# Kernel optimization log

Measured on AMD Instinct MI355X. Metric: run time of the kernel, lower is better.

Reference implementation:

```python
import jax, jax.numpy as jnp
import numpy as np

D_MODEL = 768
N_HEADS = 12
HEAD_DIM = D_MODEL // N_HEADS


def setup_inputs() -> dict:
    key = jax.random.key(0)
    ks = jax.random.split(key, 9)
    s = 1.0 / np.sqrt(D_MODEL)
    inp = {
        "inputs": jax.random.normal(ks[0], (1, 4096, D_MODEL), dtype=jnp.float32),
        "Wq": jax.random.uniform(ks[1], (D_MODEL, D_MODEL), jnp.float32, -s, s),
        "bq": jax.random.uniform(ks[2], (D_MODEL,), jnp.float32, -s, s),
        "Wk": jax.random.uniform(ks[3], (D_MODEL, D_MODEL), jnp.float32, -s, s),
        "bk": jax.random.uniform(ks[4], (D_MODEL,), jnp.float32, -s, s),
        "Wv": jax.random.uniform(ks[5], (D_MODEL, D_MODEL), jnp.float32, -s, s),
        "bv": jax.random.uniform(ks[6], (D_MODEL,), jnp.float32, -s, s),
        "Wo": jax.random.uniform(ks[7], (D_MODEL, D_MODEL), jnp.float32, -s, s),
        "bo": jax.random.uniform(ks[8], (D_MODEL,), jnp.float32, -s, s),
    }
    return inp


def reference(inputs, Wq, bq, Wk, bk, Wv, bv, Wo, bo):
    B, S, D = inputs.shape
    H, Hd = N_HEADS, HEAD_DIM

    def split_heads(x):  # [B,S,D] -> [B,H,S,Hd]
        return x.reshape(B, S, H, Hd).transpose(0, 2, 1, 3)

    # nn.Linear computes x @ W.T + b
    Q = split_heads(inputs @ Wq.T + bq)
    K = split_heads(inputs @ Wk.T + bk)
    V = split_heads(inputs @ Wv.T + bv)

    scores = jnp.einsum("bhsd,bhtd->bhst", Q, K) / jnp.sqrt(jnp.float32(Hd))
    causal = jnp.tril(jnp.ones((S, S), dtype=bool))  # True = keep
    scores = jnp.where(causal, scores, -jnp.inf)
    attn = jax.nn.softmax(scores, axis=-1)  # dropout is identity in eval

    out = jnp.einsum("bhst,bhtd->bhsd", attn, V)
    out = out.transpose(0, 2, 1, 3).reshape(B, S, D)
    return out @ Wo.T + bo
```

## Files before the change

kernel.cpp:

```cpp
#include <hip/hip_runtime.h>
#include <stdint.h>

#define SEQ 4096
#define DM 768
#define NH 12
#define HD 64

typedef unsigned short u16;
typedef short short8 __attribute__((ext_vector_type(8)));
typedef float floatx4 __attribute__((ext_vector_type(4)));
typedef u16 u16x4 __attribute__((ext_vector_type(4)));

__device__ inline u16 f2b(float f) {
  union { float f; uint32_t u; } v; v.f = f;
  uint32_t u = v.u;
  return (u16)((u + 0x7fffu + ((u >> 16) & 1u)) >> 16);
}

__device__ inline float b2f(u16 x) {
  union { uint32_t u; float f; } v; v.u = ((uint32_t)x) << 16;
  return v.f;
}

#if defined(__has_builtin)
#if __has_builtin(__builtin_amdgcn_cvt_pk_bf16_f32)
#define HAVE_PK_BF16 1
#endif
#endif

__device__ inline uint32_t pk_bf16(float a, float b) {
#ifdef HAVE_PK_BF16
  typedef __bf16 bf16x2_t __attribute__((ext_vector_type(2)));
  union { bf16x2_t v; uint32_t u; } c;
  c.v = __builtin_amdgcn_cvt_pk_bf16_f32(a, b);
  return c.u;
#else
  return (uint32_t)f2b(a) | ((uint32_t)f2b(b) << 16);
#endif
}

__device__ inline void load_lds16(const void* g, void* l) {
  __builtin_amdgcn_global_load_lds(
      (const __attribute__((address_space(1))) uint32_t*)g,
      (__attribute__((address_space(3))) uint32_t*)l, 16, 0, 0);
}

__global__ __launch_bounds__(256) void convert_all(
    const float* __restrict__ X, const float* __restrict__ Wq,
    const float* __restrict__ Wk, const float* __restrict__ Wv,
    const float* __restrict__ Wo,
    u16* __restrict__ Xb, u16* __restrict__ Wqb, u16* __restrict__ Wkb,
    u16* __restrict__ Wvb, u16* __restrict__ Wob) {
  int t = blockIdx.x * 256 + threadIdx.x;
  const int NX = SEQ * DM / 4;
  const int NW = DM * DM / 4;
  const float* src; u16* dst; int off;
  if (t < NX)               { src = X;  dst = Xb;  off = t; }
  else if (t < NX + NW)     { src = Wq; dst = Wqb; off = t - NX; }
  else if (t < NX + 2 * NW) { src = Wk; dst = Wkb; off = t - NX - NW; }
  else if (t < NX + 3 * NW) { src = Wv; dst = Wvb; off = t - NX - 2 * NW; }
  else if (t < NX + 4 * NW) { src = Wo; dst = Wob; off = t - NX - 3 * NW; }
  else return;
  float4 v = *(const float4*)(src + (size_t)off * 4);
  uint2 o;
  o.x = pk_bf16(v.x, v.y);
  o.y = pk_bf16(v.z, v.w);
  *(uint2*)(dst + (size_t)off * 4) = o;
}

__global__ __launch_bounds__(256) void gemm_qkv(
    const u16* __restrict__ Xb,
    const u16* __restrict__ Wqb, const u16* __restrict__ Wkb,
    const u16* __restrict__ Wvb,
    const float* __restrict__ bq, const float* __restrict__ bk,
    const float* __restrict__ bv,
    u16* __restrict__ Qh, u16* __restrict__ Kh, u16* __restrict__ VtG) {
  const u16* W; const float* bias;
  const int z = blockIdx.z;
  if (z == 0)      { W = Wqb; bias = bq; }
  else if (z == 1) { W = Wkb; bias = bk; }
  else             { W = Wvb; bias = bv; }

  __shared__ u16 smem[32768];

  const int tid = threadIdx.x;
  const int wave = tid >> 6, lane = tid & 63;
  const int g = lane >> 4, ln = lane & 15;
  const int m0 = blockIdx.y * 128, n0 = blockIdx.x * 128;
  const int wm = (wave & 1) * 64, wn = (wave >> 1) * 64;
  const int srow = lane >> 3;
  const int schunk = (lane & 7) ^ srow;
  const int swz = ln & 7;

  floatx4 acc[4][4] = {};

#pragma unroll
  for (int i = 0; i < 4; ++i) {
    int u = wave * 4 + i;
    load_lds16(Xb + (size_t)(m0 + u * 8 + srow) * DM + schunk * 8, smem + u * 512);
    load_lds16(W + (size_t)(n0 + u * 8 + srow) * DM + schunk * 8,
               smem + 16384 + u * 512);
  }

  for (int kt = 0; kt < 12; ++kt) {
    const int cur = kt & 1;
    __syncthreads();
    if (kt < 11) {
      const int k0 = (kt + 1) * 64, nb = cur ^ 1;
#pragma unroll
      for (int i = 0; i < 4; ++i) {
        int u = wave * 4 + i;
        load_lds16(Xb + (size_t)(m0 + u * 8 + srow) * DM + k0 + schunk * 8,
                   smem + nb * 8192 + u * 512);
        load_lds16(W + (size_t)(n0 + u * 8 + srow) * DM + k0 + schunk * 8,
                   smem + 16384 + nb * 8192 + u * 512);
      }
    }
    const u16* Ac = smem + cur * 8192;
    const u16* Bc = smem + 16384 + cur * 8192;
    short8 af[4][2], bf[4][2];
#pragma unroll
    for (int mi = 0; mi < 4; ++mi)
#pragma unroll
      for (int kh = 0; kh < 2; ++kh)
        af[mi][kh] = *(const short8*)(Ac + (wm + mi * 16 + ln) * 64 +
                                      ((kh * 4 + g) ^ swz) * 8);
#pragma unroll
    for (int ni = 0; ni < 4; ++ni)
#pragma unroll
      for (int kh = 0; kh < 2; ++kh)
        bf[ni][kh] = *(const short8*)(Bc + (wn + ni * 16 + ln) * 64 +
                                      ((kh * 4 + g) ^ swz) * 8);
#pragma unroll
    for (int kh = 0; kh < 2; ++kh)
#pragma unroll
      for (int mi = 0; mi < 4; ++mi)
#pragma unroll
        for (int ni = 0; ni < 4; ++ni)
          acc[mi][ni] = __builtin_amdgcn_mfma_f32_16x16x32_bf16(
              af[mi][kh], bf[ni][kh], acc[mi][ni], 0, 0, 0);
  }

  const float qscale = 0.125f * 1.44269504089f;
  __syncthreads();

  if (z == 2) {
#pragma unroll
    for (int mi = 0; mi < 4; ++mi) {
      int row0 = wm + mi * 16 + g * 4;
#pragma unroll
      for (int ni = 0; ni < 4; ++ni) {
        int col = wn + ni * 16 + ln;
        float b = bias[n0 + col];
        uint2 o;
        o.x = pk_bf16(acc[mi][ni][0] + b, acc[mi][ni][1] + b);
        o.y = pk_bf16(acc[mi][ni][2] + b, acc[mi][ni][3] + b);
        *(uint2*)(smem + col * 136 + row0) = o;
      }
    }
    __syncthreads();
#pragma unroll
    for (int t = 0; t < 8; ++t) {
      int unit = tid + t * 256;
      int dcol = unit >> 4, ch = unit & 15;
      short8 v = *(const short8*)(smem + dcol * 136 + ch * 8);
      int col = n0 + dcol, hh = col >> 6, dd = col & 63;
      *(short8*)(VtG + ((size_t)(hh * 64 + dd)) * SEQ + m0 + ch * 8) = v;
    }
  } else {
    u16* out = (z == 0) ? Qh : Kh;
    float cs = (z == 0) ? qscale : 1.0f;
#pragma unroll
    for (int mi = 0; mi < 4; ++mi) {
      int row0 = wm + mi * 16 + g * 4;
#pragma unroll
      for (int ni = 0; ni < 4; ++ni) {
        int col = wn + ni * 16 + ln;
        float b = bias[n0 + col];
        uint32_t w0 = pk_bf16((acc[mi][ni][0] + b) * cs, (acc[mi][ni][1] + b) * cs);
        uint32_t w1 = pk_bf16((acc[mi][ni][2] + b) * cs, (acc[mi][ni][3] + b) * cs);
        smem[(row0 + 0) * 136 + col] = (u16)w0;
        smem[(row0 + 1) * 136 + col] = (u16)(w0 >> 16);
        smem[(row0 + 2) * 136 + col] = (u16)w1;
        smem[(row0 + 3) * 136 + col] = (u16)(w1 >> 16);
      }
    }
    __syncthreads();
#pragma unroll
    for (int t = 0; t < 8; ++t) {
      int unit = tid + t * 256;
      int row = unit >> 4, ch = unit & 15;
      short8 v = *(const short8*)(smem + row * 136 + ch * 8);
      int col = n0 + ch * 8, hh = col >> 6, dd = col & 63;
      *(short8*)(out + ((size_t)hh * SEQ + m0 + row) * HD + dd) = v;
    }
  }
}

#define CHUNK 16
__global__ __launch_bounds__(256) void attn_chunk(
    const u16* __restrict__ Qh, const u16* __restrict__ Kh,
    const u16* __restrict__ VtG, u16* __restrict__ Opart,
    float2* __restrict__ Mlp) {
  const int h = blockIdx.x;
  const int b = blockIdx.y;
  int qb, ci;
  if (b < 16)      { qb = b;               ci = 0; }
  else if (b < 48) { int r = b - 16; qb = 16 + (r >> 1); ci = r & 1; }
  else if (b < 96) { int r = b - 48; int d = r / 3; qb = 32 + d; ci = r - d * 3; }
  else             { int r = b - 96; qb = 48 + (r >> 2); ci = r & 3; }
  const int kb0 = ci * CHUNK;
  const int kb1 = min(kb0 + CHUNK, qb + 1);

  const int tid = threadIdx.x, wave = tid >> 6, lane = tid & 63;
  const int g = lane >> 4, ln = lane & 15;
  const int q0 = qb * 64;
  const int srow = lane >> 3;
  const int schunk = (lane & 7) ^ srow;
  const int swz = ln & 7;

  __shared__ u16 Ks[4096];
  __shared__ u16 Vt[4096];
  __shared__ u16 Ps[4][16 * 72];

  const u16* Qbase = Qh + ((size_t)h * SEQ + q0 + wave * 16 + ln) * HD;
  short8 aq[2] = { *(const short8*)(Qbase + g * 8),
                   *(const short8*)(Qbase + 32 + g * 8) };

  floatx4 oacc[4] = {};
  float m_i = -1e30f, l_i = 0.f;
  u16* PsW = &Ps[wave][0];

  const size_t kbase = (size_t)h * SEQ * HD;
  const size_t vbase = (size_t)h * 64 * SEQ;

  for (int kb = kb0; kb < kb1; ++kb) {
    __syncthreads();
#pragma unroll
    for (int i = 0; i < 2; ++i) {
      int u = wave * 2 + i;
      load_lds16(Kh + kbase + (size_t)(kb * 64 + u * 8 + srow) * HD + schunk * 8,
                 Ks + u * 512);
      load_lds16(VtG + vbase + (size_t)(u * 8 + srow) * SEQ + kb * 64 + schunk * 8,
                 Vt + u * 512);
    }
    __syncthreads();

    floatx4 st[4] = {};
#pragma unroll
    for (int kh = 0; kh < 2; ++kh)
#pragma unroll
      for (int nt = 0; nt < 4; ++nt) {
        short8 kf = *(const short8*)(Ks + (nt * 16 + ln) * 64 +
                                     ((kh * 4 + g) ^ swz) * 8);
        st[nt] = __builtin_amdgcn_mfma_f32_16x16x32_bf16(kf, aq[kh], st[nt], 0, 0, 0);
      }

    if (kb == qb) {
      int qlocal = wave * 16 + ln;
#pragma unroll
      for (int nt = 0; nt < 4; ++nt)
#pragma unroll
        for (int r = 0; r < 4; ++r)
          if (nt * 16 + g * 4 + r > qlocal) st[nt][r] = -1e30f;
    }

    float mx = -1e30f;
#pragma unroll
    for (int nt = 0; nt < 4; ++nt)
#pragma unroll
      for (int r = 0; r < 4; ++r) mx = fmaxf(mx, st[nt][r]);
    mx = fmaxf(mx, __shfl_xor(mx, 16));
    mx = fmaxf(mx, __shfl_xor(mx, 32));
    float mnew = fmaxf(m_i, mx);
    float alpha = __builtin_amdgcn_exp2f(m_i - mnew);
    m_i = mnew;
    float rs = 0.f;
#pragma unroll
    for (int nt = 0; nt < 4; ++nt)
#pragma unroll
      for (int r = 0; r < 4; ++r) {
        float e = __builtin_amdgcn_exp2f(st[nt][r] - mnew);
        st[nt][r] = e;
        rs += e;
      }
    rs += __shfl_xor(rs, 16);
    rs += __shfl_xor(rs, 32);
    l_i = l_i * alpha + rs;
#pragma unroll
    for (int nt = 0; nt < 4; ++nt) oacc[nt] *= alpha;

#pragma unroll
    for (int nt = 0; nt < 4; ++nt) {
      uint2 pk;
      pk.x = pk_bf16(st[nt][0], st[nt][1]);
      pk.y = pk_bf16(st[nt][2], st[nt][3]);
      *(uint2*)(PsW + ln * 72 + nt * 16 + g * 4) = pk;
    }

#pragma unroll
    for (int ks = 0; ks < 2; ++ks) {
      short8 ap = *(const short8*)(PsW + ln * 72 + ks * 32 + g * 8);
#pragma unroll
      for (int nt = 0; nt < 4; ++nt) {
        short8 vf = *(const short8*)(Vt + (nt * 16 + ln) * 64 +
                                     ((ks * 4 + g) ^ swz) * 8);
        oacc[nt] = __builtin_amdgcn_mfma_f32_16x16x32_bf16(vf, ap, oacc[nt], 0, 0, 0);
      }
    }
  }

  const int slot = (h * 64 + qb) * 4 + ci;
  float inv = 1.f / l_i;
  int qloc = wave * 16 + ln;
  u16* Op = Opart + (size_t)slot * 4096 + qloc * 64;
#pragma unroll
  for (int nt = 0; nt < 4; ++nt) {
    uint2 o;
    o.x = pk_bf16(oacc[nt][0] * inv, oacc[nt][1] * inv);
    o.y = pk_bf16(oacc[nt][2] * inv, oacc[nt][3] * inv);
    *(uint2*)(Op + nt * 16 + g * 4) = o;
  }
  if (g == 0) Mlp[slot * 64 + qloc] = make_float2(m_i, l_i);
}

__global__ __launch_bounds__(256) void attn_merge(
    const u16* __restrict__ Opart, const float2* __restrict__ Mlp,
    u16* __restrict__ Ob) {
  const int h = blockIdx.x, qb = blockIdx.y;
  const int n = (qb >> 4) + 1;
  const int base = (h * 64 + qb) * 4;
  const int tid = threadIdx.x;
  const int q = tid >> 2, d0 = (tid & 3) * 16;

  float m[4], l[4];
  float M = -1e30f;
  for (int i = 0; i < n; ++i) {
    float2 ml = Mlp[(base + i) * 64 + q];
    m[i] = ml.x; l[i] = ml.y;
    M = fmaxf(M, m[i]);
  }
  float w[4], L = 0.f;
  for (int i = 0; i < n; ++i) {
    w[i] = l[i] * __builtin_amdgcn_exp2f(m[i] - M);
    L += w[i];
  }
  float invL = 1.f / L;

  float acc[16];
#pragma unroll
  for (int j = 0; j < 16; ++j) acc[j] = 0.f;
  for (int i = 0; i < n; ++i) {
    float wi = w[i] * invL;
    const u16* src = Opart + (size_t)(base + i) * 4096 + q * 64 + d0;
    short8 a = *(const short8*)(src);
    short8 b = *(const short8*)(src + 8);
#pragma unroll
    for (int j = 0; j < 8; ++j) {
      acc[j]     += wi * b2f((u16)a[j]);
      acc[8 + j] += wi * b2f((u16)b[j]);
    }
  }

  u16* dst = Ob + (size_t)(qb * 64 + q) * DM + h * HD + d0;
#pragma unroll
  for (int j = 0; j < 4; ++j) {
    uint2 o;
    o.x = pk_bf16(acc[j * 4 + 0], acc[j * 4 + 1]);
    o.y = pk_bf16(acc[j * 4 + 2], acc[j * 4 + 3]);
    *(uint2*)(dst + j * 4) = o;
  }
}

__global__ __launch_bounds__(256) void gemm_out(
    const u16* __restrict__ Ab, const u16* __restrict__ Wob,
    const float* __restrict__ bo, float* __restrict__ Cout) {
  __shared__ u16 smem[16384];

  const int tid = threadIdx.x;
  const int wave = tid >> 6, lane = tid & 63;
  const int g = lane >> 4, ln = lane & 15;
  const int m0 = blockIdx.y * 64, n0 = blockIdx.x * 64;
  const int wm = (wave & 1) * 32, wn = (wave >> 1) * 32;
  const int srow = lane >> 3;
  const int schunk = (lane & 7) ^ srow;
  const int swz = ln & 7;

  floatx4 acc[2][2] = {};

#pragma unroll
  for (int i = 0; i < 2; ++i) {
    int u = wave * 2 + i;
    load_lds16(Ab + (size_t)(m0 + u * 8 + srow) * DM + schunk * 8, smem + u * 512);
    load_lds16(Wob + (size_t)(n0 + u * 8 + srow) * DM + schunk * 8,
               smem + 8192 + u * 512);
  }

  for (int kt = 0; kt < 12; ++kt) {
    const int cur = kt & 1;
    __syncthreads();
    if (kt < 11) {
      const int k0 = (kt + 1) * 64, nb = cur ^ 1;
#pragma unroll
      for (int i = 0; i < 2; ++i) {
        int u = wave * 2 + i;
        load_lds16(Ab + (size_t)(m0 + u * 8 + srow) * DM + k0 + schunk * 8,
                   smem + nb * 4096 + u * 512);
        load_lds16(Wob + (size_t)(n0 + u * 8 + srow) * DM + k0 + schunk * 8,
                   smem + 8192 + nb * 4096 + u * 512);
      }
    }
    const u16* Ac = smem + cur * 4096;
    const u16* Bc = smem + 8192 + cur * 4096;
    short8 af[2][2], bf[2][2];
#pragma unroll
    for (int mi = 0; mi < 2; ++mi)
#pragma unroll
      for (int kh = 0; kh < 2; ++kh)
        af[mi][kh] = *(const short8*)(Ac + (wm + mi * 16 + ln) * 64 +
                                      ((kh * 4 + g) ^ swz) * 8);
#pragma unroll
    for (int ni = 0; ni < 2; ++ni)
#pragma unroll
      for (int kh = 0; kh < 2; ++kh)
        bf[ni][kh] = *(const short8*)(Bc + (wn + ni * 16 + ln) * 64 +
                                      ((kh * 4 + g) ^ swz) * 8);
#pragma unroll
    for (int kh = 0; kh < 2; ++kh)
#pragma unroll
      for (int mi = 0; mi < 2; ++mi)
#pragma unroll
        for (int ni = 0; ni < 2; ++ni)
          acc[mi][ni] = __builtin_amdgcn_mfma_f32_16x16x32_bf16(
              af[mi][kh], bf[ni][kh], acc[mi][ni], 0, 0, 0);
  }

#pragma unroll
  for (int mi = 0; mi < 2; ++mi) {
    int row = m0 + wm + mi * 16 + g * 4;
#pragma unroll
    for (int ni = 0; ni < 2; ++ni) {
      int col = n0 + wn + ni * 16 + ln;
      float b = bo[col];
#pragma unroll
      for (int r = 0; r < 4; ++r)
        Cout[(size_t)(row + r) * DM + col] = acc[mi][ni][r] + b;
    }
  }
}

extern "C" void kernel_launch(void* const* d_in, const int* in_sizes, int n_in,
                              void* d_out, int out_size, void* d_ws, size_t ws_size,
                              hipStream_t stream) {
  const float* X  = (const float*)d_in[0];
  const float* Wq = (const float*)d_in[1];
  const float* bq = (const float*)d_in[2];
  const float* Wk = (const float*)d_in[3];
  const float* bk = (const float*)d_in[4];
  const float* Wv = (const float*)d_in[5];
  const float* bv = (const float*)d_in[6];
  const float* Wo = (const float*)d_in[7];
  const float* bo = (const float*)d_in[8];
  float* out = (float*)d_out;

  char* ws = (char*)d_ws;
  u16* Xb  = (u16*)ws; ws += (size_t)SEQ * DM * 2;
  u16* Wqb = (u16*)ws; ws += (size_t)DM * DM * 2;
  u16* Wkb = (u16*)ws; ws += (size_t)DM * DM * 2;
  u16* Wvb = (u16*)ws; ws += (size_t)DM * DM * 2;
  u16* Wob = (u16*)ws; ws += (size_t)DM * DM * 2;
  u16* Qh  = (u16*)ws; ws += (size_t)NH * SEQ * HD * 2;
  u16* Kh  = (u16*)ws; ws += (size_t)NH * SEQ * HD * 2;
  u16* VtG = (u16*)ws; ws += (size_t)NH * SEQ * HD * 2;
  u16* Ob  = (u16*)ws; ws += (size_t)SEQ * DM * 2;
  u16* Opart = (u16*)ws; ws += (size_t)NH * 64 * 4 * 4096 * 2;
  float2* Mlp = (float2*)ws; ws += (size_t)NH * 64 * 4 * 64 * sizeof(float2);

  convert_all<<<5376, 256, 0, stream>>>(X, Wq, Wk, Wv, Wo, Xb, Wqb, Wkb, Wvb, Wob);

  dim3 gq(DM / 128, SEQ / 128, 3);
  gemm_qkv<<<gq, 256, 0, stream>>>(Xb, Wqb, Wkb, Wvb, bq, bk, bv, Qh, Kh, VtG);

  dim3 ga(NH, 160);
  attn_chunk<<<ga, 256, 0, stream>>>(Qh, Kh, VtG, Opart, Mlp);

  dim3 gm(NH, 64);
  attn_merge<<<gm, 256, 0, stream>>>(Opart, Mlp, Ob);

  dim3 go(DM / 64, SEQ / 64);
  gemm_out<<<go, 256, 0, stream>>>(Ob, Wob, bo, out);
}
```

Before: 194.3 us.

## Enlarge attention query tile to 128 rows with 8 waves sharing K/V tiles

The split-K attention kernel now processes 128 query rows per block with 8 waves (512 threads) instead of 64 rows with 4 waves. Each K/V tile loaded into LDS is shared by twice as many queries, so global-to-LDS traffic and block count are halved. Work chunks are now launched in reverse order, heaviest blocks first. Waves whose rows lie entirely before the current key tile skip compute but still join the barriers, so some waves idle on diagonal tiles. The merge kernel is adapted to the 128-row partial layout.

Measured after the change: 200.6 us. 3.3% more time.

```diff
diff --git a/kernel.cpp b/kernel.cpp
--- a/kernel.cpp
+++ b/kernel.cpp
@@ -198,32 +198,34 @@
 }
 
 #define CHUNK 16
-__global__ __launch_bounds__(256) void attn_chunk(
+__global__ __launch_bounds__(512, 8) void attn_chunk(
     const u16* __restrict__ Qh, const u16* __restrict__ Kh,
     const u16* __restrict__ VtG, u16* __restrict__ Opart,
     float2* __restrict__ Mlp) {
   const int h = blockIdx.x;
-  const int b = blockIdx.y;
-  int qb, ci;
-  if (b < 16)      { qb = b;               ci = 0; }
-  else if (b < 48) { int r = b - 16; qb = 16 + (r >> 1); ci = r & 1; }
-  else if (b < 96) { int r = b - 48; int d = r / 3; qb = 32 + d; ci = r - d * 3; }
-  else             { int r = b - 96; qb = 48 + (r >> 2); ci = r & 3; }
+  const int b = 79 - blockIdx.y;
+  int qB, ci;
+  if (b < 8)       { qB = b;               ci = 0; }
+  else if (b < 24) { int r = b - 8;  qB = 8 + (r >> 1); ci = r & 1; }
+  else if (b < 48) { int r = b - 24; int d = r / 3; qB = 16 + d; ci = r - d * 3; }
+  else             { int r = b - 48; qB = 24 + (r >> 2); ci = r & 3; }
   const int kb0 = ci * CHUNK;
-  const int kb1 = min(kb0 + CHUNK, qb + 1);
+  const int kb1 = min(kb0 + CHUNK, 2 * qB + 2);
 
   const int tid = threadIdx.x, wave = tid >> 6, lane = tid & 63;
   const int g = lane >> 4, ln = lane & 15;
-  const int q0 = qb * 64;
+  const int q0 = qB * 128;
+  const int qwave = q0 + wave * 16;
   const int srow = lane >> 3;
   const int schunk = (lane & 7) ^ srow;
   const int swz = ln & 7;
 
   __shared__ u16 Ks[4096];
   __shared__ u16 Vt[4096];
-  __shared__ u16 Ps[4][16 * 72];
-
-  const u16* Qbase = Qh + ((size_t)h * SEQ + q0 + wave * 16 + ln) * HD;
+  __shared__ u16 Ps[8][16 * 72];
+
+  const int qglob = qwave + ln;
+  const u16* Qbase = Qh + ((size_t)h * SEQ + qglob) * HD;
   short8 aq[2] = { *(const short8*)(Qbase + g * 8),
                    *(const short8*)(Qbase + 32 + g * 8) };
 
@@ -236,15 +238,13 @@
 
   for (int kb = kb0; kb < kb1; ++kb) {
     __syncthreads();
-#pragma unroll
-    for (int i = 0; i < 2; ++i) {
-      int u = wave * 2 + i;
-      load_lds16(Kh + kbase + (size_t)(kb * 64 + u * 8 + srow) * HD + schunk * 8,
-                 Ks + u * 512);
-      load_lds16(VtG + vbase + (size_t)(u * 8 + srow) * SEQ + kb * 64 + schunk * 8,
-                 Vt + u * 512);
-    }
-    __syncthreads();
+    load_lds16(Kh + kbase + (size_t)(kb * 64 + wave * 8 + srow) * HD + schunk * 8,
+               Ks + wave * 512);
+    load_lds16(VtG + vbase + (size_t)(wave * 8 + srow) * SEQ + kb * 64 + schunk * 8,
+               Vt + wave * 512);
+    __syncthreads();
+
+    if (kb * 64 > qwave + 15) continue;
 
     floatx4 st[4] = {};
 #pragma unroll
@@ -256,13 +256,12 @@
         st[nt] = __builtin_amdgcn_mfma_f32_16x16x32_bf16(kf, aq[kh], st[nt], 0, 0, 0);
       }
 
-    if (kb == qb) {
-      int qlocal = wave * 16 + ln;
+    if (kb * 64 + 63 > qwave) {
 #pragma unroll
       for (int nt = 0; nt < 4; ++nt)
 #pragma unroll
         for (int r = 0; r < 4; ++r)
-          if (nt * 16 + g * 4 + r > qlocal) st[nt][r] = -1e30f;
+          if (kb * 64 + nt * 16 + g * 4 + r > qglob) st[nt][r] = -1e30f;
     }
 
     float mx = -1e30f;
@@ -310,10 +309,10 @@
     }
   }
 
-  const int slot = (h * 64 + qb) * 4 + ci;
+  const int slot = (h * 32 + qB) * 4 + ci;
   float inv = 1.f / l_i;
   int qloc = wave * 16 + ln;
-  u16* Op = Opart + (size_t)slot * 4096 + qloc * 64;
+  u16* Op = Opart + (size_t)slot * 8192 + qloc * 64;
 #pragma unroll
   for (int nt = 0; nt < 4; ++nt) {
     uint2 o;
@@ -321,22 +320,22 @@
     o.y = pk_bf16(oacc[nt][2] * inv, oacc[nt][3] * inv);
     *(uint2*)(Op + nt * 16 + g * 4) = o;
   }
-  if (g == 0) Mlp[slot * 64 + qloc] = make_float2(m_i, l_i);
+  if (g == 0) Mlp[(size_t)slot * 128 + qloc] = make_float2(m_i, l_i);
 }
 
 __global__ __launch_bounds__(256) void attn_merge(
     const u16* __restrict__ Opart, const float2* __restrict__ Mlp,
     u16* __restrict__ Ob) {
-  const int h = blockIdx.x, qb = blockIdx.y;
-  const int n = (qb >> 4) + 1;
-  const int base = (h * 64 + qb) * 4;
-  const int tid = threadIdx.x;
-  const int q = tid >> 2, d0 = (tid & 3) * 16;
+  const int h = blockIdx.x, qB = blockIdx.y;
+  const int n = (qB >> 3) + 1;
+  const int base = (h * 32 + qB) * 4;
+  const int q = threadIdx.x >> 1;
+  const int d0 = (threadIdx.x & 1) * 32;
 
   float m[4], l[4];
   float M = -1e30f;
   for (int i = 0; i < n; ++i) {
-    float2 ml = Mlp[(base + i) * 64 + q];
+    float2 ml = Mlp[(size_t)(base + i) * 128 + q];
     m[i] = ml.x; l[i] = ml.y;
     M = fmaxf(M, m[i]);
   }
@@ -347,28 +346,29 @@
   }
   float invL = 1.f / L;
 
-  float acc[16];
-#pragma unroll
-  for (int j = 0; j < 16; ++j) acc[j] = 0.f;
+  float acc[32];
+#pragma unroll
+  for (int j = 0; j < 32; ++j) acc[j] = 0.f;
   for (int i = 0; i < n; ++i) {
     float wi = w[i] * invL;
-    const u16* src = Opart + (size_t)(base + i) * 4096 + q * 64 + d0;
-    short8 a = *(const short8*)(src);
-    short8 b = *(const short8*)(src + 8);
-#pragma unroll
-    for (int j = 0; j < 8; ++j) {
-      acc[j]     += wi * b2f((u16)a[j]);
-      acc[8 + j] += wi * b2f((u16)b[j]);
-    }
-  }
-
-  u16* dst = Ob + (size_t)(qb * 64 + q) * DM + h * HD + d0;
-#pragma unroll
-  for (int j = 0; j < 4; ++j) {
-    uint2 o;
-    o.x = pk_bf16(acc[j * 4 + 0], acc[j * 4 + 1]);
-    o.y = pk_bf16(acc[j * 4 + 2], acc[j * 4 + 3]);
-    *(uint2*)(dst + j * 4) = o;
+    const u16* src = Opart + (size_t)(base + i) * 8192 + q * 64 + d0;
+#pragma unroll
+    for (int c = 0; c < 4; ++c) {
+      short8 a = ((const short8*)src)[c];
+#pragma unroll
+      for (int j = 0; j < 8; ++j) acc[c * 8 + j] += wi * b2f((u16)a[j]);
+    }
+  }
+
+  u16* dst = Ob + (size_t)(qB * 128 + q) * DM + h * HD + d0;
+#pragma unroll
+  for (int c = 0; c < 4; ++c) {
+    uint4 o;
+    o.x = pk_bf16(acc[c * 8 + 0], acc[c * 8 + 1]);
+    o.y = pk_bf16(acc[c * 8 + 2], acc[c * 8 + 3]);
+    o.z = pk_bf16(acc[c * 8 + 4], acc[c * 8 + 5]);
+    o.w = pk_bf16(acc[c * 8 + 6], acc[c * 8 + 7]);
+    ((uint4*)dst)[c] = o;
   }
 }
 
@@ -473,18 +473,18 @@
   u16* Kh  = (u16*)ws; ws += (size_t)NH * SEQ * HD * 2;
   u16* VtG = (u16*)ws; ws += (size_t)NH * SEQ * HD * 2;
   u16* Ob  = (u16*)ws; ws += (size_t)SEQ * DM * 2;
-  u16* Opart = (u16*)ws; ws += (size_t)NH * 64 * 4 * 4096 * 2;
-  float2* Mlp = (float2*)ws; ws += (size_t)NH * 64 * 4 * 64 * sizeof(float2);
+  u16* Opart = (u16*)ws; ws += (size_t)NH * 32 * 4 * 128 * 64 * 2;
+  float2* Mlp = (float2*)ws; ws += (size_t)NH * 32 * 4 * 128 * sizeof(float2);
 
   convert_all<<<5376, 256, 0, stream>>>(X, Wq, Wk, Wv, Wo, Xb, Wqb, Wkb, Wvb, Wob);
 
   dim3 gq(DM / 128, SEQ / 128, 3);
   gemm_qkv<<<gq, 256, 0, stream>>>(Xb, Wqb, Wkb, Wvb, bq, bk, bv, Qh, Kh, VtG);
 
-  dim3 ga(NH, 160);
-  attn_chunk<<<ga, 256, 0, stream>>>(Qh, Kh, VtG, Opart, Mlp);
-
-  dim3 gm(NH, 64);
+  dim3 ga(NH, 80);
+  attn_chunk<<<ga, 512, 0, stream>>>(Qh, Kh, VtG, Opart, Mlp);
+
+  dim3 gm(NH, 32);
   attn_merge<<<gm, 256, 0, stream>>>(Opart, Mlp, Ob);
 
   dim3 go(DM / 64, SEQ / 64);
```
